# Optimization experiments

Hardware: AMD Instinct MI355X
Metric: run time of the kernel (lower is better)

Reference implementation:

```python
import jax, jax.numpy as jnp
import numpy as np

N = 50000      # nodes
E = 800000     # edges
IN = 128       # in_channels
C = 32         # hidden_channels per head
H = 8          # heads
NC = 2         # num_classes
EPS = 1e-5     # batchnorm eps
SLOPE = 0.2    # leaky relu negative slope


def setup_inputs() -> dict:
    key = jax.random.key(0)
    ks = jax.random.split(key, 16)
    d = {}
    d["x"] = jax.random.normal(ks[0], (N, IN), dtype=jnp.float32)
    d["edge_index"] = jax.random.randint(ks[1], (2, E), 0, N, dtype=jnp.int64)
    # layer 0: IN -> H*C (concat)
    s0 = 1.0 / np.sqrt(IN)
    d["Wl0"] = jax.random.normal(ks[2], (IN, H * C), dtype=jnp.float32) * s0
    d["Wr0"] = jax.random.normal(ks[3], (IN, H * C), dtype=jnp.float32) * s0
    d["att0"] = jax.random.normal(ks[4], (H, C), dtype=jnp.float32) * (1.0 / np.sqrt(C))
    d["b0"] = jnp.zeros((H * C,), dtype=jnp.float32)
    d["g0"] = jnp.ones((H * C,), dtype=jnp.float32)
    d["be0"] = jnp.zeros((H * C,), dtype=jnp.float32)
    d["m0"] = jax.random.normal(ks[5], (H * C,), dtype=jnp.float32) * 0.1
    d["v0"] = jax.random.uniform(ks[6], (H * C,), dtype=jnp.float32, minval=0.5, maxval=1.5)
    # layer 1: H*C -> C (mean over heads, concat=False)
    s1 = 1.0 / np.sqrt(H * C)
    d["Wl1"] = jax.random.normal(ks[7], (H * C, H * C), dtype=jnp.float32) * s1
    d["Wr1"] = jax.random.normal(ks[8], (H * C, H * C), dtype=jnp.float32) * s1
    d["att1"] = jax.random.normal(ks[9], (H, C), dtype=jnp.float32) * (1.0 / np.sqrt(C))
    d["b1"] = jnp.zeros((C,), dtype=jnp.float32)
    d["g1"] = jnp.ones((C,), dtype=jnp.float32)
    d["be1"] = jnp.zeros((C,), dtype=jnp.float32)
    d["m1"] = jax.random.normal(ks[10], (C,), dtype=jnp.float32) * 0.1
    d["v1"] = jax.random.uniform(ks[11], (C,), dtype=jnp.float32, minval=0.5, maxval=1.5)
    # classifier C -> NC
    d["Wc"] = jax.random.normal(ks[12], (C, NC), dtype=jnp.float32) * (1.0 / np.sqrt(C))
    d["bc"] = jnp.zeros((NC,), dtype=jnp.float32)
    return d


def _gatv2_layer(x, src, dst, Wl, Wr, att, b, concat, num_nodes):
    # GATv2Conv (PyG semantics): x_l = source proj, x_r = target proj,
    # e_ij = att . LeakyReLU(x_l[j] + x_r[i]); softmax over incoming edges of i;
    # out_i = sum_j alpha_ij * x_l[j]. Self-loops are added (PyG default).
    nH, nC = att.shape
    xl = (x @ Wl).reshape(num_nodes, nH, nC)
    xr = (x @ Wr).reshape(num_nodes, nH, nC)
    e = xl[src] + xr[dst]                              # [E', H, C]
    e = jnp.where(e > 0, e, SLOPE * e)
    logits = jnp.einsum('ehc,hc->eh', e, att)          # [E', H]
    m = jax.ops.segment_max(logits, dst, num_segments=num_nodes)   # [N, H]
    ex = jnp.exp(logits - m[dst])
    denom = jax.ops.segment_sum(ex, dst, num_segments=num_nodes)   # [N, H]
    alpha = ex / denom[dst]                            # [E', H]
    msg = alpha[:, :, None] * xl[src]                  # [E', H, C]
    out = jax.ops.segment_sum(msg, dst, num_segments=num_nodes)    # [N, H, C]
    if concat:
        return out.reshape(num_nodes, nH * nC) + b
    return out.mean(axis=1) + b


def _bn(x, g, be, m, v):
    return (x - m) * jax.lax.rsqrt(v + EPS) * g + be


def reference(x, edge_index, Wl0, Wr0, att0, b0, g0, be0, m0, v0,
              Wl1, Wr1, att1, b1, g1, be1, m1, v1, Wc, bc):
    num_nodes = x.shape[0]
    loop = jnp.arange(num_nodes, dtype=edge_index.dtype)
    src = jnp.concatenate([edge_index[0], loop])
    dst = jnp.concatenate([edge_index[1], loop])
    h = _gatv2_layer(x, src, dst, Wl0, Wr0, att0, b0, True, num_nodes)
    h = _bn(h, g0, be0, m0, v0)
    h = jax.nn.elu(h)   # eval mode: dropout is identity
    h = _gatv2_layer(h, src, dst, Wl1, Wr1, att1, b1, False, num_nodes)
    h = _bn(h, g1, be1, m1, v1)
    return h @ Wc + bc
```

## Files before the change

### kernel.cpp

```cpp
#include <hip/hip_runtime.h>
#include <math.h>

#define N_NODES 50000
#define M_PAD   50048
#define E_EDGES 800000
#define IN_CH   128
#define C_CH    32
#define H_HEADS 8
#define HC      256
#define BN_EPS  1e-5f
#define SLOPE   0.2f
#define LOG2E   1.44269504f

#define SCAN_CHUNK 512
#define SCAN_B     ((N_NODES + SCAN_CHUNK - 1) / SCAN_CHUNK)

#define EDGE_BLOCKS 2048
#define EDGE_WAVES  (EDGE_BLOCKS * 4)

typedef _Float16 f16x8 __attribute__((ext_vector_type(8)));
typedef _Float16 f16x4 __attribute__((ext_vector_type(4)));
typedef _Float16 f16x2 __attribute__((ext_vector_type(2)));
typedef float    f32x4 __attribute__((ext_vector_type(4)));

#if __has_builtin(__builtin_amdgcn_exp2f)
#define EXP2F(x) __builtin_amdgcn_exp2f(x)
#else
#define EXP2F(x) exp2f(x)
#endif


__global__ void k_init_deg(int* deg, int n) {
    int i = blockIdx.x * blockDim.x + threadIdx.x;
    if (i < n) deg[i] = 1;
}

__global__ void k_hist(const int* __restrict__ dst, int* deg, int e) {
    int i = blockIdx.x * blockDim.x + threadIdx.x;
    if (i < e) atomicAdd(&deg[dst[i]], 1);
}

__global__ __launch_bounds__(256) void k_scan_local(
        const int* __restrict__ deg, int* __restrict__ row_ptr,
        int* __restrict__ partials, int n) {
    __shared__ int sm[256];
    int t = threadIdx.x;
    int base = blockIdx.x * SCAN_CHUNK;
    int i0 = base + 2 * t, i1 = i0 + 1;
    int a = (i0 < n) ? deg[i0] : 0;
    int b = (i1 < n) ? deg[i1] : 0;
    int s = a + b;
    sm[t] = s;
    __syncthreads();
    #pragma unroll
    for (int off = 1; off < 256; off <<= 1) {
        int u = (t >= off) ? sm[t - off] : 0;
        __syncthreads();
        sm[t] += u;
        __syncthreads();
    }
    int excl = sm[t] - s;
    if (i0 < n) row_ptr[i0] = excl;
    if (i1 < n) row_ptr[i1] = excl + a;
    if (t == 255) partials[blockIdx.x] = sm[255];
}

__global__ __launch_bounds__(128) void k_scan_part(
        int* __restrict__ partials, int* __restrict__ row_ptr_n) {
    __shared__ int sm[128];
    int t = threadIdx.x;
    int v = (t < SCAN_B) ? partials[t] : 0;
    sm[t] = v;
    __syncthreads();
    #pragma unroll
    for (int off = 1; off < 128; off <<= 1) {
        int u = (t >= off) ? sm[t - off] : 0;
        __syncthreads();
        sm[t] += u;
        __syncthreads();
    }
    if (t < SCAN_B) partials[t] = sm[t] - v;
    if (t == 127) *row_ptr_n = sm[127];
}

__global__ void k_scan_add(int* __restrict__ row_ptr, int* __restrict__ cursor,
                           const int* __restrict__ partials, int n) {
    int i = blockIdx.x * blockDim.x + threadIdx.x;
    if (i < n) {
        int v = row_ptr[i] + partials[i / SCAN_CHUNK];
        row_ptr[i] = v;
        cursor[i] = v;
    }
}

__global__ void k_fill(const int* __restrict__ src, const int* __restrict__ dst,
                       int* cursor, int* csr_src, int e, int n) {
    int i = blockIdx.x * blockDim.x + threadIdx.x;
    if (i < e) {
        int d = dst[i];
        int p = atomicAdd(&cursor[d], 1);
        csr_src[p] = src[i];
    } else if (i < e + n) {
        int v = i - e;
        int p = atomicAdd(&cursor[v], 1);
        csr_src[p] = v;
    }
}


__global__ void k_split_w4(const float* __restrict__ Wl0, const float* __restrict__ Wr0,
                           const float* __restrict__ Wl1, const float* __restrict__ Wr1,
                           _Float16* __restrict__ W0lt, _Float16* __restrict__ W0rt,
                           _Float16* __restrict__ W1lt, _Float16* __restrict__ W1rt) {
    int t = blockIdx.x * blockDim.x + threadIdx.x;
    const float* W; _Float16* O; int K, rel;
    if (t < 32768)       { W = Wl0; O = W0lt; K = 128; rel = t; }
    else if (t < 65536)  { W = Wr0; O = W0rt; K = 128; rel = t - 32768; }
    else if (t < 131072) { W = Wl1; O = W1lt; K = 256; rel = t - 65536; }
    else if (t < 196608) { W = Wr1; O = W1rt; K = 256; rel = t - 131072; }
    else return;
    int n = rel / K, k = rel - n * K;
    O[rel] = (_Float16)W[(size_t)k * 256 + n];
}


#define BK  32
#define LDA 40

__device__ __forceinline__ f16x8 cvt_h8(float4 a, float4 b) {
    f16x8 v = { (_Float16)a.x, (_Float16)a.y, (_Float16)a.z, (_Float16)a.w,
                (_Float16)b.x, (_Float16)b.y, (_Float16)b.z, (_Float16)b.w };
    return v;
}

__global__ __launch_bounds__(512) void k_gemm_mfma(
        const _Float16* __restrict__ A16, const float* __restrict__ A32,
        const _Float16* __restrict__ W0t, const _Float16* __restrict__ W1t,
        _Float16* __restrict__ C0, _Float16* __restrict__ C1, int K) {
    __shared__ _Float16 As [128 * LDA];
    __shared__ _Float16 Bs0[128 * LDA];
    __shared__ _Float16 Bs1[128 * LDA];
    int t = threadIdx.x;
    int lane = t & 63, wv = t >> 6;
    int quad = lane >> 4, r16 = lane & 15;
    size_t mBase = (size_t)blockIdx.x * 128;
    size_t nBase = (size_t)blockIdx.y * 128;
    int sr = t >> 2;
    int sc = (t & 3) * 8;
    f32x4 acc0[8] = {}, acc1[8] = {};
    for (int k0 = 0; k0 < K; k0 += BK) {
        if (A32) {
            size_t r0 = mBase + sr;
            float4 a0 = {0.f, 0.f, 0.f, 0.f}, a1 = a0;
            if (r0 < N_NODES) {
                const float* g = A32 + r0 * K + k0 + sc;
                a0 = ((const float4*)g)[0];
                a1 = ((const float4*)g)[1];
            }
            *(f16x8*)&As[sr * LDA + sc] = cvt_h8(a0, a1);
        } else {
            *(f16x8*)&As[sr * LDA + sc] =
                *(const f16x8*)(A16 + (size_t)(mBase + sr) * K + k0 + sc);
        }
        *(f16x8*)&Bs0[sr * LDA + sc] = *(const f16x8*)(W0t + (size_t)(nBase + sr) * K + k0 + sc);
        *(f16x8*)&Bs1[sr * LDA + sc] = *(const f16x8*)(W1t + (size_t)(nBase + sr) * K + k0 + sc);
        __syncthreads();
        f16x8 av = *(f16x8*)&As[(wv * 16 + r16) * LDA + quad * 8];
        #pragma unroll
        for (int ni = 0; ni < 8; ++ni) {
            f16x8 bv0 = *(f16x8*)&Bs0[(ni * 16 + r16) * LDA + quad * 8];
            f16x8 bv1 = *(f16x8*)&Bs1[(ni * 16 + r16) * LDA + quad * 8];
            acc0[ni] = __builtin_amdgcn_mfma_f32_16x16x32_f16(av, bv0, acc0[ni], 0, 0, 0);
            acc1[ni] = __builtin_amdgcn_mfma_f32_16x16x32_f16(av, bv1, acc1[ni], 0, 0, 0);
        }
        __syncthreads();
    }
    #pragma unroll
    for (int r = 0; r < 4; ++r) {
        size_t row = mBase + wv * 16 + quad * 4 + r;
        _Float16* cp0 = C0 + row * 256 + nBase + r16;
        _Float16* cp1 = C1 + row * 256 + nBase + r16;
        #pragma unroll
        for (int ni = 0; ni < 8; ++ni) {
            cp0[ni * 16] = (_Float16)acc0[ni][r];
            cp1[ni * 16] = (_Float16)acc1[ni][r];
        }
    }
}


__device__ __forceinline__ float edge_w16(f16x4 h, f16x4 xr, f16x4 att) {
    f16x4 e = h + xr;
    f16x4 es = e * (_Float16)SLOPE;
    f16x4 l = __builtin_elementwise_max(e, es);
#if __has_builtin(__builtin_amdgcn_fdot2)
    f16x2 l01 = __builtin_shufflevector(l, l, 0, 1);
    f16x2 l23 = __builtin_shufflevector(l, l, 2, 3);
    f16x2 a01 = __builtin_shufflevector(att, att, 0, 1);
    f16x2 a23 = __builtin_shufflevector(att, att, 2, 3);
    float p = __builtin_amdgcn_fdot2(l01, a01, 0.f, false);
    p = __builtin_amdgcn_fdot2(l23, a23, p, false);
#else
    float p = (float)l[0] * (float)att[0];
    p = fmaf((float)l[1], (float)att[1], p);
    p = fmaf((float)l[2], (float)att[2], p);
    p = fmaf((float)l[3], (float)att[3], p);
#endif
    p += __shfl_xor(p, 1);
    p += __shfl_xor(p, 2);
    p += __shfl_xor(p, 4);
    return EXP2F(p);
}

__device__ __forceinline__ float4 edge_accum(
        const f16x4* __restrict__ xlp, f16x4 xr_h, f16x4 att_h,
        const int* __restrict__ csr_src, int beg, int end) {
    float4 acc = {0.f, 0.f, 0.f, 0.f};
    float S = 0.f;
    int j = beg;
    for (; j + 4 <= end; j += 4) {
        int s0 = csr_src[j];
        int s1 = csr_src[j + 1];
        int s2 = csr_src[j + 2];
        int s3 = csr_src[j + 3];
        f16x4 h0 = xlp[(size_t)s0 * 64];
        f16x4 h1 = xlp[(size_t)s1 * 64];
        f16x4 h2 = xlp[(size_t)s2 * 64];
        f16x4 h3 = xlp[(size_t)s3 * 64];
        float w0 = edge_w16(h0, xr_h, att_h);
        float w1 = edge_w16(h1, xr_h, att_h);
        float w2 = edge_w16(h2, xr_h, att_h);
        float w3 = edge_w16(h3, xr_h, att_h);
        S += (w0 + w1) + (w2 + w3);
        acc.x = fmaf((float)h0[0], w0, acc.x); acc.y = fmaf((float)h0[1], w0, acc.y);
        acc.z = fmaf((float)h0[2], w0, acc.z); acc.w = fmaf((float)h0[3], w0, acc.w);
        acc.x = fmaf((float)h1[0], w1, acc.x); acc.y = fmaf((float)h1[1], w1, acc.y);
        acc.z = fmaf((float)h1[2], w1, acc.z); acc.w = fmaf((float)h1[3], w1, acc.w);
        acc.x = fmaf((float)h2[0], w2, acc.x); acc.y = fmaf((float)h2[1], w2, acc.y);
        acc.z = fmaf((float)h2[2], w2, acc.z); acc.w = fmaf((float)h2[3], w2, acc.w);
        acc.x = fmaf((float)h3[0], w3, acc.x); acc.y = fmaf((float)h3[1], w3, acc.y);
        acc.z = fmaf((float)h3[2], w3, acc.z); acc.w = fmaf((float)h3[3], w3, acc.w);
    }
    for (; j < end; ++j) {
        int s = csr_src[j];
        f16x4 hv = xlp[(size_t)s * 64];
        float w = edge_w16(hv, xr_h, att_h);
        S += w;
        acc.x = fmaf((float)hv[0], w, acc.x); acc.y = fmaf((float)hv[1], w, acc.y);
        acc.z = fmaf((float)hv[2], w, acc.z); acc.w = fmaf((float)hv[3], w, acc.w);
    }
    float inv = 1.f / S;
    acc.x *= inv; acc.y *= inv; acc.z *= inv; acc.w *= inv;
    return acc;
}

__global__ __launch_bounds__(256) void k_edge0(
        const _Float16* __restrict__ xl, const _Float16* __restrict__ xr,
        const float* __restrict__ att,
        const int* __restrict__ row_ptr, const int* __restrict__ csr_src,
        const float* __restrict__ b0, const float* __restrict__ g0,
        const float* __restrict__ be0, const float* __restrict__ m0,
        const float* __restrict__ v0,
        _Float16* __restrict__ h0) {
    int lane = threadIdx.x & 63;
    const f16x4* xlp = (const f16x4*)xl + lane;
    float4 af = ((const float4*)att)[lane];
    f16x4 att_h = { (_Float16)(af.x * LOG2E), (_Float16)(af.y * LOG2E),
                    (_Float16)(af.z * LOG2E), (_Float16)(af.w * LOG2E) };
    float4 bb = ((const float4*)b0)[lane];
    float4 gg = ((const float4*)g0)[lane];
    float4 ee = ((const float4*)be0)[lane];
    float4 mm = ((const float4*)m0)[lane];
    float4 vv = ((const float4*)v0)[lane];
    float4 sc, sh;
    sc.x = rsqrtf(vv.x + BN_EPS) * gg.x;  sh.x = (bb.x - mm.x) * sc.x + ee.x;
    sc.y = rsqrtf(vv.y + BN_EPS) * gg.y;  sh.y = (bb.y - mm.y) * sc.y + ee.y;
    sc.z = rsqrtf(vv.z + BN_EPS) * gg.z;  sh.z = (bb.z - mm.z) * sc.z + ee.z;
    sc.w = rsqrtf(vv.w + BN_EPS) * gg.w;  sh.w = (bb.w - mm.w) * sc.w + ee.w;
    int w = blockIdx.x * 4 + (threadIdx.x >> 6);
    for (int i0 = w; i0 < N_NODES; i0 += EDGE_WAVES) {
        int i = __builtin_amdgcn_readfirstlane(i0);
        f16x4 xr_h = ((const f16x4*)xr)[(size_t)i * 64 + lane];
        int beg = row_ptr[i], end = row_ptr[i + 1];
        float4 r = edge_accum(xlp, xr_h, att_h, csr_src, beg, end);
        float4 o;
        o.x = r.x * sc.x + sh.x;
        o.y = r.y * sc.y + sh.y;
        o.z = r.z * sc.z + sh.z;
        o.w = r.w * sc.w + sh.w;
        o.x = o.x > 0.f ? o.x : expm1f(o.x);
        o.y = o.y > 0.f ? o.y : expm1f(o.y);
        o.z = o.z > 0.f ? o.z : expm1f(o.z);
        o.w = o.w > 0.f ? o.w : expm1f(o.w);
        f16x4 hh = { (_Float16)o.x, (_Float16)o.y, (_Float16)o.z, (_Float16)o.w };
        ((f16x4*)h0)[(size_t)i * 64 + lane] = hh;
    }
}

__global__ __launch_bounds__(256) void k_edge1(
        const _Float16* __restrict__ xl, const _Float16* __restrict__ xr,
        const float* __restrict__ att,
        const int* __restrict__ row_ptr, const int* __restrict__ csr_src,
        const float* __restrict__ b1, const float* __restrict__ g1,
        const float* __restrict__ be1, const float* __restrict__ m1,
        const float* __restrict__ v1,
        const float* __restrict__ Wc, const float* __restrict__ bc,
        float* __restrict__ out) {
    int lane = threadIdx.x & 63;
    int q = lane & 7;
    const f16x4* xlp = (const f16x4*)xl + lane;
    float4 af = ((const float4*)att)[lane];
    f16x4 att_h = { (_Float16)(af.x * LOG2E), (_Float16)(af.y * LOG2E),
                    (_Float16)(af.z * LOG2E), (_Float16)(af.w * LOG2E) };
    float4 bb = ((const float4*)b1)[q];
    float4 gg = ((const float4*)g1)[q];
    float4 ee = ((const float4*)be1)[q];
    float4 mm = ((const float4*)m1)[q];
    float4 vv = ((const float4*)v1)[q];
    float4 sA, sB;
    {
        float s;
        s = rsqrtf(vv.x + BN_EPS) * gg.x; sA.x = 0.125f * s; sB.x = (bb.x - mm.x) * s + ee.x;
        s = rsqrtf(vv.y + BN_EPS) * gg.y; sA.y = 0.125f * s; sB.y = (bb.y - mm.y) * s + ee.y;
        s = rsqrtf(vv.z + BN_EPS) * gg.z; sA.z = 0.125f * s; sB.z = (bb.z - mm.z) * s + ee.z;
        s = rsqrtf(vv.w + BN_EPS) * gg.w; sA.w = 0.125f * s; sB.w = (bb.w - mm.w) * s + ee.w;
    }
    float4 wc0 = ((const float4*)Wc)[q * 2];
    float4 wc1 = ((const float4*)Wc)[q * 2 + 1];
    float bc0 = bc[0], bc1 = bc[1];
    int w = blockIdx.x * 4 + (threadIdx.x >> 6);
    for (int i0 = w; i0 < N_NODES; i0 += EDGE_WAVES) {
        int i = __builtin_amdgcn_readfirstlane(i0);
        f16x4 xr_h = ((const f16x4*)xr)[(size_t)i * 64 + lane];
        int beg = row_ptr[i], end = row_ptr[i + 1];
        float4 r = edge_accum(xlp, xr_h, att_h, csr_src, beg, end);
        #pragma unroll
        for (int mask = 8; mask <= 32; mask <<= 1) {
            r.x += __shfl_xor(r.x, mask);
            r.y += __shfl_xor(r.y, mask);
            r.z += __shfl_xor(r.z, mask);
            r.w += __shfl_xor(r.w, mask);
        }
        float4 o;
        o.x = r.x * sA.x + sB.x;
        o.y = r.y * sA.y + sB.y;
        o.z = r.z * sA.z + sB.z;
        o.w = r.w * sA.w + sB.w;
        float o0 = o.x * wc0.x + o.y * wc0.z + o.z * wc1.x + o.w * wc1.z;
        float o1 = o.x * wc0.y + o.y * wc0.w + o.z * wc1.y + o.w * wc1.w;
        #pragma unroll
        for (int mask = 1; mask <= 4; mask <<= 1) {
            o0 += __shfl_xor(o0, mask);
            o1 += __shfl_xor(o1, mask);
        }
        if (lane == 0) {
            float2 ov = {o0 + bc0, o1 + bc1};
            *(float2*)(out + (size_t)i * 2) = ov;
        }
    }
}


extern "C" void kernel_launch(void* const* d_in, const int* in_sizes, int n_in,
                              void* d_out, int out_size, void* d_ws, size_t ws_size,
                              hipStream_t stream) {
    const float* x    = (const float*)d_in[0];
    const int*   ei   = (const int*)d_in[1];
    const float* Wl0  = (const float*)d_in[2];
    const float* Wr0  = (const float*)d_in[3];
    const float* att0 = (const float*)d_in[4];
    const float* b0   = (const float*)d_in[5];
    const float* g0   = (const float*)d_in[6];
    const float* be0  = (const float*)d_in[7];
    const float* m0   = (const float*)d_in[8];
    const float* v0   = (const float*)d_in[9];
    const float* Wl1  = (const float*)d_in[10];
    const float* Wr1  = (const float*)d_in[11];
    const float* att1 = (const float*)d_in[12];
    const float* b1   = (const float*)d_in[13];
    const float* g1   = (const float*)d_in[14];
    const float* be1  = (const float*)d_in[15];
    const float* m1   = (const float*)d_in[16];
    const float* v1   = (const float*)d_in[17];
    const float* Wc   = (const float*)d_in[18];
    const float* bc   = (const float*)d_in[19];
    float* out = (float*)d_out;

    const int N = N_NODES, E = E_EDGES;
    const int* srcp = ei;
    const int* dstp = ei + E;

    char* p = (char*)d_ws;
    _Float16* xlf = (_Float16*)p; p += (size_t)M_PAD * HC * 2;
    _Float16* xrf = (_Float16*)p; p += (size_t)M_PAD * HC * 2;
    _Float16* h0  = (_Float16*)p; p += (size_t)M_PAD * HC * 2;
    _Float16* W0lt = (_Float16*)p; p += (size_t)HC * IN_CH * 2;
    _Float16* W0rt = (_Float16*)p; p += (size_t)HC * IN_CH * 2;
    _Float16* W1lt = (_Float16*)p; p += (size_t)HC * HC * 2;
    _Float16* W1rt = (_Float16*)p; p += (size_t)HC * HC * 2;
    int* deg      = (int*)p;
    int* row_ptr  = deg + N;
    int* cursor   = row_ptr + (N + 1);
    int* partials = cursor + N;
    int* csr_src  = partials + ((SCAN_B + 3) & ~3);

    k_init_deg<<<(N + 255) / 256, 256, 0, stream>>>(deg, N);
    k_hist<<<(E + 255) / 256, 256, 0, stream>>>(dstp, deg, E);
    k_scan_local<<<SCAN_B, 256, 0, stream>>>(deg, row_ptr, partials, N);
    k_scan_part<<<1, 128, 0, stream>>>(partials, row_ptr + N);
    k_scan_add<<<(N + 255) / 256, 256, 0, stream>>>(row_ptr, cursor, partials, N);
    k_fill<<<(E + N + 255) / 256, 256, 0, stream>>>(srcp, dstp, cursor, csr_src, E, N);

    k_split_w4<<<768, 256, 0, stream>>>(Wl0, Wr0, Wl1, Wr1, W0lt, W0rt, W1lt, W1rt);

    dim3 ggrid(M_PAD / 128, 2);
    k_gemm_mfma<<<ggrid, 512, 0, stream>>>(nullptr, x, W0lt, W0rt, xlf, xrf, IN_CH);
    k_edge0<<<EDGE_BLOCKS, 256, 0, stream>>>(xlf, xrf, att0, row_ptr, csr_src,
                                             b0, g0, be0, m0, v0, h0);
    k_gemm_mfma<<<ggrid, 512, 0, stream>>>(h0, nullptr, W1lt, W1rt, xlf, xrf, HC);
    k_edge1<<<EDGE_BLOCKS, 256, 0, stream>>>(xlf, xrf, att1, row_ptr, csr_src,
                                             b1, g1, be1, m1, v1, Wc, bc, out);
}
```

Measured before the change: 418.5 us.

## Launch one wave per node, pre-scale CSR offsets, use DPP quad reductions

Edge kernels drop the grid-stride loop and launch one wavefront per node (N/4 blocks), so the per-node prologue moves inside each wave. CSR source indices are stored pre-shifted by 9 as byte offsets into the fp16 row, which removes the 64-bit multiply per gathered row. The first two butterfly steps of the 8-lane dot-product reduction use DPP quad permutes instead of ds_swizzle/bpermute shuffles. In exchange, per-wave parameter loads and BN constants are recomputed for every node, and the byte offset limits how many nodes the int32 index can address.

Result: faster. 387.7 us (-7.4%).

```diff
diff --git a/kernel.cpp b/kernel.cpp
--- a/kernel.cpp
+++ b/kernel.cpp
@@ -14,9 +14,6 @@
 
 #define SCAN_CHUNK 512
 #define SCAN_B     ((N_NODES + SCAN_CHUNK - 1) / SCAN_CHUNK)
-
-#define EDGE_BLOCKS 2048
-#define EDGE_WAVES  (EDGE_BLOCKS * 4)
 
 typedef _Float16 f16x8 __attribute__((ext_vector_type(8)));
 typedef _Float16 f16x4 __attribute__((ext_vector_type(4)));
@@ -99,11 +96,11 @@
     if (i < e) {
         int d = dst[i];
         int p = atomicAdd(&cursor[d], 1);
-        csr_src[p] = src[i];
+        csr_src[p] = src[i] << 9;
     } else if (i < e + n) {
         int v = i - e;
         int p = atomicAdd(&cursor[v], 1);
-        csr_src[p] = v;
+        csr_src[p] = v << 9;
     }
 }
 
@@ -189,6 +186,20 @@
 }
 
 
+__device__ __forceinline__ float qreduce8(float p) {
+#if __has_builtin(__builtin_amdgcn_mov_dpp)
+    p += __builtin_bit_cast(float, __builtin_amdgcn_mov_dpp(
+             __builtin_bit_cast(int, p), 0xB1, 0xF, 0xF, true));
+    p += __builtin_bit_cast(float, __builtin_amdgcn_mov_dpp(
+             __builtin_bit_cast(int, p), 0x4E, 0xF, 0xF, true));
+#else
+    p += __shfl_xor(p, 1);
+    p += __shfl_xor(p, 2);
+#endif
+    p += __shfl_xor(p, 4);
+    return p;
+}
+
 __device__ __forceinline__ float edge_w16(f16x4 h, f16x4 xr, f16x4 att) {
     f16x4 e = h + xr;
     f16x4 es = e * (_Float16)SLOPE;
@@ -206,27 +217,24 @@
     p = fmaf((float)l[2], (float)att[2], p);
     p = fmaf((float)l[3], (float)att[3], p);
 #endif
-    p += __shfl_xor(p, 1);
-    p += __shfl_xor(p, 2);
-    p += __shfl_xor(p, 4);
-    return EXP2F(p);
+    return EXP2F(qreduce8(p));
 }
 
 __device__ __forceinline__ float4 edge_accum(
-        const f16x4* __restrict__ xlp, f16x4 xr_h, f16x4 att_h,
+        const char* __restrict__ xlb, f16x4 xr_h, f16x4 att_h,
         const int* __restrict__ csr_src, int beg, int end) {
     float4 acc = {0.f, 0.f, 0.f, 0.f};
     float S = 0.f;
     int j = beg;
     for (; j + 4 <= end; j += 4) {
-        int s0 = csr_src[j];
-        int s1 = csr_src[j + 1];
-        int s2 = csr_src[j + 2];
-        int s3 = csr_src[j + 3];
-        f16x4 h0 = xlp[(size_t)s0 * 64];
-        f16x4 h1 = xlp[(size_t)s1 * 64];
-        f16x4 h2 = xlp[(size_t)s2 * 64];
-        f16x4 h3 = xlp[(size_t)s3 * 64];
+        int o0 = csr_src[j];
+        int o1 = csr_src[j + 1];
+        int o2 = csr_src[j + 2];
+        int o3 = csr_src[j + 3];
+        f16x4 h0 = *(const f16x4*)(xlb + o0);
+        f16x4 h1 = *(const f16x4*)(xlb + o1);
+        f16x4 h2 = *(const f16x4*)(xlb + o2);
+        f16x4 h3 = *(const f16x4*)(xlb + o3);
         float w0 = edge_w16(h0, xr_h, att_h);
         float w1 = edge_w16(h1, xr_h, att_h);
         float w2 = edge_w16(h2, xr_h, att_h);
@@ -242,8 +250,8 @@
         acc.z = fmaf((float)h3[2], w3, acc.z); acc.w = fmaf((float)h3[3], w3, acc.w);
     }
     for (; j < end; ++j) {
-        int s = csr_src[j];
-        f16x4 hv = xlp[(size_t)s * 64];
+        int o = csr_src[j];
+        f16x4 hv = *(const f16x4*)(xlb + o);
         float w = edge_w16(hv, xr_h, att_h);
         S += w;
         acc.x = fmaf((float)hv[0], w, acc.x); acc.y = fmaf((float)hv[1], w, acc.y);
@@ -263,38 +271,30 @@
         const float* __restrict__ v0,
         _Float16* __restrict__ h0) {
     int lane = threadIdx.x & 63;
-    const f16x4* xlp = (const f16x4*)xl + lane;
+    int i = __builtin_amdgcn_readfirstlane(blockIdx.x * 4 + (threadIdx.x >> 6));
+    const char* xlb = (const char*)xl + lane * 8;
+    f16x4 xr_h = ((const f16x4*)xr)[(size_t)i * 64 + lane];
     float4 af = ((const float4*)att)[lane];
     f16x4 att_h = { (_Float16)(af.x * LOG2E), (_Float16)(af.y * LOG2E),
                     (_Float16)(af.z * LOG2E), (_Float16)(af.w * LOG2E) };
+    int beg = row_ptr[i], end = row_ptr[i + 1];
+    float4 r = edge_accum(xlb, xr_h, att_h, csr_src, beg, end);
     float4 bb = ((const float4*)b0)[lane];
     float4 gg = ((const float4*)g0)[lane];
     float4 ee = ((const float4*)be0)[lane];
     float4 mm = ((const float4*)m0)[lane];
     float4 vv = ((const float4*)v0)[lane];
-    float4 sc, sh;
-    sc.x = rsqrtf(vv.x + BN_EPS) * gg.x;  sh.x = (bb.x - mm.x) * sc.x + ee.x;
-    sc.y = rsqrtf(vv.y + BN_EPS) * gg.y;  sh.y = (bb.y - mm.y) * sc.y + ee.y;
-    sc.z = rsqrtf(vv.z + BN_EPS) * gg.z;  sh.z = (bb.z - mm.z) * sc.z + ee.z;
-    sc.w = rsqrtf(vv.w + BN_EPS) * gg.w;  sh.w = (bb.w - mm.w) * sc.w + ee.w;
-    int w = blockIdx.x * 4 + (threadIdx.x >> 6);
-    for (int i0 = w; i0 < N_NODES; i0 += EDGE_WAVES) {
-        int i = __builtin_amdgcn_readfirstlane(i0);
-        f16x4 xr_h = ((const f16x4*)xr)[(size_t)i * 64 + lane];
-        int beg = row_ptr[i], end = row_ptr[i + 1];
-        float4 r = edge_accum(xlp, xr_h, att_h, csr_src, beg, end);
-        float4 o;
-        o.x = r.x * sc.x + sh.x;
-        o.y = r.y * sc.y + sh.y;
-        o.z = r.z * sc.z + sh.z;
-        o.w = r.w * sc.w + sh.w;
-        o.x = o.x > 0.f ? o.x : expm1f(o.x);
-        o.y = o.y > 0.f ? o.y : expm1f(o.y);
-        o.z = o.z > 0.f ? o.z : expm1f(o.z);
-        o.w = o.w > 0.f ? o.w : expm1f(o.w);
-        f16x4 hh = { (_Float16)o.x, (_Float16)o.y, (_Float16)o.z, (_Float16)o.w };
-        ((f16x4*)h0)[(size_t)i * 64 + lane] = hh;
-    }
+    float4 o;
+    o.x = (r.x + bb.x - mm.x) * rsqrtf(vv.x + BN_EPS) * gg.x + ee.x;
+    o.y = (r.y + bb.y - mm.y) * rsqrtf(vv.y + BN_EPS) * gg.y + ee.y;
+    o.z = (r.z + bb.z - mm.z) * rsqrtf(vv.z + BN_EPS) * gg.z + ee.z;
+    o.w = (r.w + bb.w - mm.w) * rsqrtf(vv.w + BN_EPS) * gg.w + ee.w;
+    o.x = o.x > 0.f ? o.x : expm1f(o.x);
+    o.y = o.y > 0.f ? o.y : expm1f(o.y);
+    o.z = o.z > 0.f ? o.z : expm1f(o.z);
+    o.w = o.w > 0.f ? o.w : expm1f(o.w);
+    f16x4 hh = { (_Float16)o.x, (_Float16)o.y, (_Float16)o.z, (_Float16)o.w };
+    ((f16x4*)h0)[(size_t)i * 64 + lane] = hh;
 }
 
 __global__ __launch_bounds__(256) void k_edge1(
@@ -308,55 +308,42 @@
         float* __restrict__ out) {
     int lane = threadIdx.x & 63;
     int q = lane & 7;
-    const f16x4* xlp = (const f16x4*)xl + lane;
+    int i = __builtin_amdgcn_readfirstlane(blockIdx.x * 4 + (threadIdx.x >> 6));
+    const char* xlb = (const char*)xl + lane * 8;
+    f16x4 xr_h = ((const f16x4*)xr)[(size_t)i * 64 + lane];
     float4 af = ((const float4*)att)[lane];
     f16x4 att_h = { (_Float16)(af.x * LOG2E), (_Float16)(af.y * LOG2E),
                     (_Float16)(af.z * LOG2E), (_Float16)(af.w * LOG2E) };
+    int beg = row_ptr[i], end = row_ptr[i + 1];
+    float4 r = edge_accum(xlb, xr_h, att_h, csr_src, beg, end);
+    #pragma unroll
+    for (int mask = 8; mask <= 32; mask <<= 1) {
+        r.x += __shfl_xor(r.x, mask);
+        r.y += __shfl_xor(r.y, mask);
+        r.z += __shfl_xor(r.z, mask);
+        r.w += __shfl_xor(r.w, mask);
+    }
     float4 bb = ((const float4*)b1)[q];
     float4 gg = ((const float4*)g1)[q];
     float4 ee = ((const float4*)be1)[q];
     float4 mm = ((const float4*)m1)[q];
     float4 vv = ((const float4*)v1)[q];
-    float4 sA, sB;
-    {
-        float s;
-        s = rsqrtf(vv.x + BN_EPS) * gg.x; sA.x = 0.125f * s; sB.x = (bb.x - mm.x) * s + ee.x;
-        s = rsqrtf(vv.y + BN_EPS) * gg.y; sA.y = 0.125f * s; sB.y = (bb.y - mm.y) * s + ee.y;
-        s = rsqrtf(vv.z + BN_EPS) * gg.z; sA.z = 0.125f * s; sB.z = (bb.z - mm.z) * s + ee.z;
-        s = rsqrtf(vv.w + BN_EPS) * gg.w; sA.w = 0.125f * s; sB.w = (bb.w - mm.w) * s + ee.w;
-    }
+    r.x = (r.x * 0.125f + bb.x - mm.x) * rsqrtf(vv.x + BN_EPS) * gg.x + ee.x;
+    r.y = (r.y * 0.125f + bb.y - mm.y) * rsqrtf(vv.y + BN_EPS) * gg.y + ee.y;
+    r.z = (r.z * 0.125f + bb.z - mm.z) * rsqrtf(vv.z + BN_EPS) * gg.z + ee.z;
+    r.w = (r.w * 0.125f + bb.w - mm.w) * rsqrtf(vv.w + BN_EPS) * gg.w + ee.w;
     float4 wc0 = ((const float4*)Wc)[q * 2];
     float4 wc1 = ((const float4*)Wc)[q * 2 + 1];
-    float bc0 = bc[0], bc1 = bc[1];
-    int w = blockIdx.x * 4 + (threadIdx.x >> 6);
-    for (int i0 = w; i0 < N_NODES; i0 += EDGE_WAVES) {
-        int i = __builtin_amdgcn_readfirstlane(i0);
-        f16x4 xr_h = ((const f16x4*)xr)[(size_t)i * 64 + lane];
-        int beg = row_ptr[i], end = row_ptr[i + 1];
-        float4 r = edge_accum(xlp, xr_h, att_h, csr_src, beg, end);
-        #pragma unroll
-        for (int mask = 8; mask <= 32; mask <<= 1) {
-            r.x += __shfl_xor(r.x, mask);
-            r.y += __shfl_xor(r.y, mask);
-            r.z += __shfl_xor(r.z, mask);
-            r.w += __shfl_xor(r.w, mask);
-        }
-        float4 o;
-        o.x = r.x * sA.x + sB.x;
-        o.y = r.y * sA.y + sB.y;
-        o.z = r.z * sA.z + sB.z;
-        o.w = r.w * sA.w + sB.w;
-        float o0 = o.x * wc0.x + o.y * wc0.z + o.z * wc1.x + o.w * wc1.z;
-        float o1 = o.x * wc0.y + o.y * wc0.w + o.z * wc1.y + o.w * wc1.w;
-        #pragma unroll
-        for (int mask = 1; mask <= 4; mask <<= 1) {
-            o0 += __shfl_xor(o0, mask);
-            o1 += __shfl_xor(o1, mask);
-        }
-        if (lane == 0) {
-            float2 ov = {o0 + bc0, o1 + bc1};
-            *(float2*)(out + (size_t)i * 2) = ov;
-        }
+    float o0 = r.x * wc0.x + r.y * wc0.z + r.z * wc1.x + r.w * wc1.z;
+    float o1 = r.x * wc0.y + r.y * wc0.w + r.z * wc1.y + r.w * wc1.w;
+    #pragma unroll
+    for (int mask = 1; mask <= 4; mask <<= 1) {
+        o0 += __shfl_xor(o0, mask);
+        o1 += __shfl_xor(o1, mask);
+    }
+    if (lane == 0) {
+        float2 ov = {o0 + bc[0], o1 + bc[1]};
+        *(float2*)(out + (size_t)i * 2) = ov;
     }
 }
 
@@ -415,9 +402,9 @@
 
     dim3 ggrid(M_PAD / 128, 2);
     k_gemm_mfma<<<ggrid, 512, 0, stream>>>(nullptr, x, W0lt, W0rt, xlf, xrf, IN_CH);
-    k_edge0<<<EDGE_BLOCKS, 256, 0, stream>>>(xlf, xrf, att0, row_ptr, csr_src,
-                                             b0, g0, be0, m0, v0, h0);
+    k_edge0<<<N / 4, 256, 0, stream>>>(xlf, xrf, att0, row_ptr, csr_src,
+                                       b0, g0, be0, m0, v0, h0);
     k_gemm_mfma<<<ggrid, 512, 0, stream>>>(h0, nullptr, W1lt, W1rt, xlf, xrf, HC);
-    k_edge1<<<EDGE_BLOCKS, 256, 0, stream>>>(xlf, xrf, att1, row_ptr, csr_src,
-                                             b1, g1, be1, m1, v1, Wc, bc, out);
-}
+    k_edge1<<<N / 4, 256, 0, stream>>>(xlf, xrf, att1, row_ptr, csr_src,
+                                       b1, g1, be1, m1, v1, Wc, bc, out);
+}
```
